# Performance work log

Hardware: AMD Instinct MI355X
Metric: run time of the kernel (lower is better)

The kernel has to match this reference:

```python
import jax, jax.numpy as jnp
import numpy as np

N_NODES = 50000
N_HYPEREDGES = 50000
E = 320000
D = 256


def _prelu(x, a):
    return jnp.where(x >= 0, x, a * x)


def _hypergraph_conv(x, hei, W, b, num_nodes, num_edges):
    # PyG HypergraphConv, use_attention=False, heads=1:
    # out = D^{-1} H B^{-1} H^T (X W^T) + b
    src = hei[0]  # node indices, [E]
    he = hei[1]   # hyperedge indices, [E]
    xw = x @ W.T  # [N, D] node transform (lin has no bias)
    ones = jnp.ones((hei.shape[1],), x.dtype)
    deg_n = jax.ops.segment_sum(ones, src, num_segments=num_nodes)   # node degree D
    deg_e = jax.ops.segment_sum(ones, he, num_segments=num_edges)    # hyperedge size B
    d_inv = jnp.where(deg_n > 0, 1.0 / deg_n, 0.0)
    b_inv = jnp.where(deg_e > 0, 1.0 / deg_e, 0.0)
    # node -> hyperedge aggregation, scaled by B^{-1}
    edge_feat = b_inv[:, None] * jax.ops.segment_sum(xw[src], he, num_segments=num_edges)  # [n_he, D]
    # hyperedge -> node aggregation, scaled by D^{-1}
    out = d_inv[:, None] * jax.ops.segment_sum(edge_feat[he], src, num_segments=num_nodes)  # [N, D]
    return out + b


def setup_inputs() -> dict:
    key = jax.random.key(0)
    ks = jax.random.split(key, 6)
    std = np.sqrt(2.0 / D)  # kaiming_normal
    x = jax.random.normal(ks[0], (N_NODES, D), dtype=jnp.float32)
    hyper_edge_index = jax.random.randint(ks[1], (2, E), 0, N_HYPEREDGES, dtype=jnp.int64)
    W1 = jax.random.normal(ks[2], (D, D), dtype=jnp.float32) * std
    b1 = jnp.zeros((D,), jnp.float32)
    W2 = jax.random.normal(ks[3], (D, D), dtype=jnp.float32) * std
    b2 = jnp.zeros((D,), jnp.float32)
    prelu_a = jnp.asarray(0.25, jnp.float32)
    return {"x": x, "W1": W1, "b1": b1, "W2": W2, "b2": b2,
            "prelu_a": prelu_a, "hyper_edge_index": hyper_edge_index}


def reference(x, W1, b1, W2, b2, prelu_a, hyper_edge_index):
    out = _hypergraph_conv(x, hyper_edge_index, W1, b1, N_NODES, N_HYPEREDGES)
    out = _prelu(out, prelu_a)
    out = _hypergraph_conv(out, hyper_edge_index, W2, b2, N_NODES, N_HYPEREDGES)
    out = out + x  # residual
    out = _prelu(out, prelu_a)
    return out
```

## Files before the change

kernel.cpp:

```cpp
#include <hip/hip_runtime.h>

#define NN    50000
#define NHE   50000
#define NEDGE 320000
#define DD    256

#define SB    1024
#define NBLK  ((NN + SB - 1) / SB)
#define CNTB  ((NEDGE / 4 + 255) / 256)
#define FB    ((NEDGE / 4 + 1023) / 1024)

typedef float f32x4 __attribute__((ext_vector_type(4)));
typedef short short8 __attribute__((ext_vector_type(8)));

static __device__ __forceinline__ unsigned short f2b(float f) {
    union { float f; unsigned u; } c; c.f = f;
    unsigned u = c.u;
    u += 0x7fffu + ((u >> 16) & 1u);
    return (unsigned short)(u >> 16);
}
static __device__ __forceinline__ float b2f_lo(unsigned v) {
    union { unsigned u; float f; } c; c.u = v << 16; return c.f;
}
static __device__ __forceinline__ float b2f_hi(unsigned v) {
    union { unsigned u; float f; } c; c.u = v & 0xffff0000u; return c.f;
}
static __device__ __forceinline__ unsigned pack2(float a, float b) {
    return (unsigned)f2b(a) | ((unsigned)f2b(b) << 16);
}

static __device__ __forceinline__ void glds16(const unsigned short* g, unsigned short* l) {
    __builtin_amdgcn_global_load_lds((const __attribute__((address_space(1))) unsigned int*)g,
                                     (__attribute__((address_space(3))) unsigned int*)l,
                                     16, 0, 0);
}

__global__ __launch_bounds__(256) void k_count_cvt(const int* __restrict__ src,
                                                   const int* __restrict__ he,
                                                   int* __restrict__ cnt_n,
                                                   int* __restrict__ cnt_e,
                                                   int* __restrict__ rank_n,
                                                   int* __restrict__ rank_e,
                                                   const float* __restrict__ w1,
                                                   const float* __restrict__ w2,
                                                   unsigned short* __restrict__ o1,
                                                   unsigned short* __restrict__ o2) {
    int bx = blockIdx.x;
    if (bx >= CNTB) {
        int t = (bx - CNTB) * 256 + threadIdx.x;
        const int n4 = DD * DD / 4;
        const float* s = (t < n4) ? w1 : w2;
        unsigned short* d = (t < n4) ? o1 : o2;
        int i = (t < n4) ? t : t - n4;
        float4 v = ((const float4*)s)[i];
        uint2 o;
        o.x = pack2(v.x, v.y);
        o.y = pack2(v.z, v.w);
        ((uint2*)d)[i] = o;
        return;
    }
    int t  = bx * 256 + threadIdx.x;
    int e0 = t * 4;
    if (e0 >= NEDGE) return;
    int4 s = *(const int4*)(src + e0);
    int4 h = *(const int4*)(he + e0);
    int4 rn, re;
    rn.x = atomicAdd(&cnt_n[s.x], 1);
    rn.y = atomicAdd(&cnt_n[s.y], 1);
    rn.z = atomicAdd(&cnt_n[s.z], 1);
    rn.w = atomicAdd(&cnt_n[s.w], 1);
    re.x = atomicAdd(&cnt_e[h.x], 1);
    re.y = atomicAdd(&cnt_e[h.y], 1);
    re.z = atomicAdd(&cnt_e[h.z], 1);
    re.w = atomicAdd(&cnt_e[h.w], 1);
    *(int4*)(rank_n + e0) = rn;
    *(int4*)(rank_e + e0) = re;
}

__global__ __launch_bounds__(256) void k_scan(const int* __restrict__ cnt_n,
                                              const int* __restrict__ cnt_e,
                                              int* __restrict__ off_n,
                                              int* __restrict__ off_e) {
    int b   = blockIdx.x;
    int seg = b / NBLK, lb = b % NBLK;
    const int* cnt = seg ? cnt_e : cnt_n;
    int* off = seg ? off_e : off_n;
    int t = threadIdx.x;

    int pre = lb * SB;
    int s = 0;
    for (int i = t * 4; i < pre; i += 1024) {
        int4 c = *(const int4*)(cnt + i);
        s += c.x + c.y + c.z + c.w;
    }
    __shared__ int red[256];
    red[t] = s;
    __syncthreads();
    for (int o = 128; o > 0; o >>= 1) {
        if (t < o) red[t] += red[t + o];
        __syncthreads();
    }
    int base = red[0];

    int idx = pre + t * 4;
    int v[4];
    int tsum = 0;
#pragma unroll
    for (int j = 0; j < 4; ++j) {
        v[j] = (idx + j < NN) ? cnt[idx + j] : 0;
        tsum += v[j];
    }
    __shared__ int sc[256];
    sc[t] = tsum;
    __syncthreads();
    for (int o = 1; o < 256; o <<= 1) {
        int val = (t >= o) ? sc[t - o] : 0;
        __syncthreads();
        sc[t] += val;
        __syncthreads();
    }
    int p = base + sc[t] - tsum;
#pragma unroll
    for (int j = 0; j < 4; ++j) {
        if (idx + j < NN) off[idx + j] = p;
        p += v[j];
    }
    if (lb == NBLK - 1 && t == 255) off[NN] = base + sc[255];
}

template <bool A32>
static __device__ __forceinline__ void gemm_bres_body(const void* __restrict__ Av,
                                                      const unsigned short* __restrict__ Wb,
                                                      unsigned short* __restrict__ Cb,
                                                      int bid) {
    __shared__ __align__(16) unsigned short Bs[128 * 256];
    const int t    = threadIdx.x;
    const int lane = t & 63;
    const int wave = t >> 6;
    const int n0   = (bid & 1) * 128;

#pragma unroll
    for (int q = 0; q < 4; ++q) {
        int row   = q * 32 + wave * 2 + (lane >> 5);
        int chunk = lane & 31;
        glds16(Wb + (size_t)(n0 + row) * DD + ((chunk ^ (row & 7)) * 8),
               Bs + q * 8192 + wave * 512);
    }
    __syncthreads();

    const int fr = lane & 15;
    const int fq = lane >> 4;
    int chunk = (bid >> 1) * 16 + wave;
    if (chunk * 16 >= NN) return;
    int m0 = chunk * 16;

    f32x4 acc[8] = {};
    short8 af[8];
    if (A32) {
        const float* p = (const float*)Av + (size_t)(m0 + fr) * DD + fq * 8;
#pragma unroll
        for (int kc = 0; kc < 8; ++kc) {
            const float* pp = p + kc * 32;
            float4 f0 = ((const float4*)pp)[0];
            float4 f1 = ((const float4*)pp)[1];
            uint4 u;
            u.x = pack2(f0.x, f0.y); u.y = pack2(f0.z, f0.w);
            u.z = pack2(f1.x, f1.y); u.w = pack2(f1.z, f1.w);
            af[kc] = *(short8*)&u;
        }
    } else {
        const unsigned short* p = (const unsigned short*)Av + (size_t)(m0 + fr) * DD + fq * 8;
#pragma unroll
        for (int kc = 0; kc < 8; ++kc)
            af[kc] = *(const short8*)(p + kc * 32);
    }

#pragma unroll
    for (int kc = 0; kc < 8; ++kc) {
#pragma unroll
        for (int nt = 0; nt < 8; ++nt) {
            int r  = nt * 16 + fr;
            int ch = (kc * 4 + fq) ^ (fr & 7);
            short8 bf = *(const short8*)(Bs + r * 256 + ch * 8);
            acc[nt] = __builtin_amdgcn_mfma_f32_16x16x32_bf16(af[kc], bf, acc[nt], 0, 0, 0);
        }
    }

#pragma unroll
    for (int nt = 0; nt < 8; ++nt)
#pragma unroll
        for (int i = 0; i < 4; ++i)
            Cb[(size_t)(m0 + fq * 4 + i) * DD + n0 + nt * 16 + fr] = f2b(acc[nt][i]);
}

__global__ __launch_bounds__(1024) void k_fill_gemm1(const int* __restrict__ src,
                                                     const int* __restrict__ he,
                                                     const int* __restrict__ off_n,
                                                     const int* __restrict__ off_e,
                                                     const int* __restrict__ rank_n,
                                                     const int* __restrict__ rank_e,
                                                     int* __restrict__ adj_n,
                                                     int* __restrict__ adj_e,
                                                     const float* __restrict__ x,
                                                     const unsigned short* __restrict__ w1b,
                                                     unsigned short* __restrict__ B1) {
    int bx = blockIdx.x;
    if (bx < FB) {
        int t  = bx * 1024 + threadIdx.x;
        int e0 = t * 4;
        if (e0 >= NEDGE) return;
        int4 s  = *(const int4*)(src + e0);
        int4 h  = *(const int4*)(he + e0);
        int4 rn = *(const int4*)(rank_n + e0);
        int4 re = *(const int4*)(rank_e + e0);
        int on0 = off_n[s.x], on1 = off_n[s.y], on2 = off_n[s.z], on3 = off_n[s.w];
        int oe0 = off_e[h.x], oe1 = off_e[h.y], oe2 = off_e[h.z], oe3 = off_e[h.w];
        adj_n[on0 + rn.x] = h.x;
        adj_n[on1 + rn.y] = h.y;
        adj_n[on2 + rn.z] = h.z;
        adj_n[on3 + rn.w] = h.w;
        adj_e[oe0 + re.x] = s.x;
        adj_e[oe1 + re.y] = s.y;
        adj_e[oe2 + re.z] = s.z;
        adj_e[oe3 + re.w] = s.w;
        return;
    }
    gemm_bres_body<true>((const void*)x, w1b, B1, bx - FB);
}

__global__ __launch_bounds__(1024) void k_gemm2(const unsigned short* __restrict__ Av,
                                                const unsigned short* __restrict__ Wb,
                                                unsigned short* __restrict__ Cb) {
    gemm_bres_body<false>((const void*)Av, Wb, Cb, blockIdx.x);
}

static __device__ __forceinline__ void acc8(float* a, uint4 v) {
    a[0] += b2f_lo(v.x); a[1] += b2f_hi(v.x);
    a[2] += b2f_lo(v.y); a[3] += b2f_hi(v.y);
    a[4] += b2f_lo(v.z); a[5] += b2f_hi(v.z);
    a[6] += b2f_lo(v.w); a[7] += b2f_hi(v.w);
}
static __device__ __forceinline__ void gather8(const unsigned short* __restrict__ srcb,
                                               const int* __restrict__ adj,
                                               int b, int e, int sl, float* a) {
#pragma unroll
    for (int i = 0; i < 8; ++i) a[i] = 0.f;
    for (int i = b; i < e; i += 8) {
        int g0 = adj[i];
        int g[8];
        g[0] = g0;
#pragma unroll
        for (int j = 1; j < 8; ++j) g[j] = (i + j < e) ? adj[i + j] : g0;
        uint4 v[8];
#pragma unroll
        for (int j = 0; j < 8; ++j)
            v[j] = *(const uint4*)(srcb + (size_t)g[j] * DD + sl * 8);
        acc8(a, v[0]);
#pragma unroll
        for (int j = 1; j < 8; ++j)
            if (i + j < e) acc8(a, v[j]);
    }
}

__global__ __launch_bounds__(256) void k_gather_edge_b(const unsigned short* __restrict__ xw,
                                                       unsigned short* __restrict__ ef,
                                                       const int* __restrict__ off,
                                                       const int* __restrict__ adj) {
    int tid = blockIdx.x * 256 + threadIdx.x;
    int w = tid >> 5;
    int sl = tid & 31;
    if (w >= NHE) return;
    int b = off[w], e = off[w + 1];
    float a[8];
    gather8(xw, adj, b, e, sl, a);
    float sc = (e > b) ? 1.f / (float)(e - b) : 0.f;
    uint4 o;
    o.x = pack2(a[0] * sc, a[1] * sc);
    o.y = pack2(a[2] * sc, a[3] * sc);
    o.z = pack2(a[4] * sc, a[5] * sc);
    o.w = pack2(a[6] * sc, a[7] * sc);
    *(uint4*)(ef + (size_t)w * DD + sl * 8) = o;
}

__global__ __launch_bounds__(256) void k_gather_node_mid_b(const unsigned short* __restrict__ ef,
                                                           unsigned short* __restrict__ h,
                                                           const int* __restrict__ off,
                                                           const int* __restrict__ adj,
                                                           const float* __restrict__ bias,
                                                           const float* __restrict__ aP) {
    int tid = blockIdx.x * 256 + threadIdx.x;
    int w = tid >> 5;
    int sl = tid & 31;
    if (w >= NN) return;
    int b = off[w], e = off[w + 1];
    float a[8];
    gather8(ef, adj, b, e, sl, a);
    float sc = (e > b) ? 1.f / (float)(e - b) : 0.f;
    float al = *aP;
    float4 bb0 = ((const float4*)bias)[sl * 2];
    float4 bb1 = ((const float4*)bias)[sl * 2 + 1];
    float r[8];
    r[0] = a[0] * sc + bb0.x; r[1] = a[1] * sc + bb0.y;
    r[2] = a[2] * sc + bb0.z; r[3] = a[3] * sc + bb0.w;
    r[4] = a[4] * sc + bb1.x; r[5] = a[5] * sc + bb1.y;
    r[6] = a[6] * sc + bb1.z; r[7] = a[7] * sc + bb1.w;
#pragma unroll
    for (int i = 0; i < 8; ++i) r[i] = (r[i] >= 0.f) ? r[i] : al * r[i];
    uint4 o;
    o.x = pack2(r[0], r[1]);
    o.y = pack2(r[2], r[3]);
    o.z = pack2(r[4], r[5]);
    o.w = pack2(r[6], r[7]);
    *(uint4*)(h + (size_t)w * DD + sl * 8) = o;
}

__global__ __launch_bounds__(256) void k_gather_node_final_b(const unsigned short* __restrict__ ef,
                                                             const float* __restrict__ x,
                                                             float* __restrict__ out,
                                                             const int* __restrict__ off,
                                                             const int* __restrict__ adj,
                                                             const float* __restrict__ bias,
                                                             const float* __restrict__ aP) {
    int tid = blockIdx.x * 256 + threadIdx.x;
    int w = tid >> 5;
    int sl = tid & 31;
    if (w >= NN) return;
    int b = off[w], e = off[w + 1];
    float a[8];
    gather8(ef, adj, b, e, sl, a);
    float sc = (e > b) ? 1.f / (float)(e - b) : 0.f;
    float al = *aP;
    float4 bb0 = ((const float4*)bias)[sl * 2];
    float4 bb1 = ((const float4*)bias)[sl * 2 + 1];
    const float* xp = x + (size_t)w * DD + sl * 8;
    float4 xv0 = *(const float4*)xp;
    float4 xv1 = *(const float4*)(xp + 4);
    float r[8];
    r[0] = a[0] * sc + bb0.x + xv0.x; r[1] = a[1] * sc + bb0.y + xv0.y;
    r[2] = a[2] * sc + bb0.z + xv0.z; r[3] = a[3] * sc + bb0.w + xv0.w;
    r[4] = a[4] * sc + bb1.x + xv1.x; r[5] = a[5] * sc + bb1.y + xv1.y;
    r[6] = a[6] * sc + bb1.z + xv1.z; r[7] = a[7] * sc + bb1.w + xv1.w;
#pragma unroll
    for (int i = 0; i < 8; ++i) r[i] = (r[i] >= 0.f) ? r[i] : al * r[i];
    float* op = out + (size_t)w * DD + sl * 8;
    *(float4*)op = make_float4(r[0], r[1], r[2], r[3]);
    *(float4*)(op + 4) = make_float4(r[4], r[5], r[6], r[7]);
}

extern "C" void kernel_launch(void* const* d_in, const int* in_sizes, int n_in,
                              void* d_out, int out_size, void* d_ws, size_t ws_size,
                              hipStream_t stream) {
    const float* x       = (const float*)d_in[0];
    const float* W1      = (const float*)d_in[1];
    const float* b1      = (const float*)d_in[2];
    const float* W2      = (const float*)d_in[3];
    const float* b2      = (const float*)d_in[4];
    const float* prelu_a = (const float*)d_in[5];
    const int*   hei     = (const int*)d_in[6];
    const int* idx_src = hei;
    const int* idx_he  = hei + NEDGE;

    float* out = (float*)d_out;
    unsigned short* B1 = (unsigned short*)d_ws;
    unsigned short* B2 = B1 + (size_t)NN * DD;
    int* off_n  = (int*)(B2 + (size_t)NN * DD);
    int* off_e  = off_n + NN + 1;
    int* cnt_n  = off_e + NHE + 1;
    int* cnt_e  = cnt_n + NN;
    int* adj_n  = cnt_e + NHE;
    int* adj_e  = adj_n + NEDGE;
    int* rank_n = adj_e + NEDGE;
    int* rank_e = rank_n + NEDGE;
    unsigned short* w1b = (unsigned short*)d_out;
    unsigned short* w2b = w1b + DD * DD;

    const int gblocks = (NN * 32 + 255) / 256;
    const int gemmb   = 2 * ((NN / 16 + 15) / 16);

    hipMemsetAsync(cnt_n, 0, sizeof(int) * (NN + NHE), stream);
    k_count_cvt<<<CNTB + 128, 256, 0, stream>>>(idx_src, idx_he, cnt_n, cnt_e,
                                                rank_n, rank_e, W1, W2, w1b, w2b);
    k_scan<<<2 * NBLK, 256, 0, stream>>>(cnt_n, cnt_e, off_n, off_e);

    k_fill_gemm1<<<FB + gemmb, 1024, 0, stream>>>(idx_src, idx_he, off_n, off_e,
                                                  rank_n, rank_e, adj_n, adj_e,
                                                  x, w1b, B1);
    k_gather_edge_b<<<gblocks, 256, 0, stream>>>(B1, B2, off_e, adj_e);
    k_gather_node_mid_b<<<gblocks, 256, 0, stream>>>(B2, B1, off_n, adj_n, b1, prelu_a);

    k_gemm2<<<gemmb, 1024, 0, stream>>>(B1, w2b, B2);
    k_gather_edge_b<<<gblocks, 256, 0, stream>>>(B2, B1, off_e, adj_e);
    k_gather_node_final_b<<<gblocks, 256, 0, stream>>>(B1, x, out, off_n, adj_n, b2, prelu_a);
}
```

Baseline: 312.7 us.

## Move x bf16 conversion into count kernel and split fill from GEMM1

The fp32-to-bf16 conversion of x now runs as extra blocks of the counting kernel, writing into the B2 workspace, so GEMM1 reads bf16 A like GEMM2 and one GEMM kernel serves both layers. The adjacency fill becomes its own 256-thread kernel instead of sharing a 1024-thread launch with GEMM1. The GEMM now issues its A-fragment loads before the LDS barrier and clamps the last row chunk so those loads stay in bounds. This adds a kernel launch and an extra pass writing and reading bf16 x, and gives up the old overlap of the fill work with GEMM1.

New measurement: 306.4 us. -2.0%, faster.

```diff
diff --git a/kernel.cpp b/kernel.cpp
--- a/kernel.cpp
+++ b/kernel.cpp
@@ -8,7 +8,7 @@
 #define SB    1024
 #define NBLK  ((NN + SB - 1) / SB)
 #define CNTB  ((NEDGE / 4 + 255) / 256)
-#define FB    ((NEDGE / 4 + 1023) / 1024)
+#define XCB   (NN * DD / 2048)
 
 typedef float f32x4 __attribute__((ext_vector_type(4)));
 typedef short short8 __attribute__((ext_vector_type(8)));
@@ -44,8 +44,20 @@
                                                    const float* __restrict__ w1,
                                                    const float* __restrict__ w2,
                                                    unsigned short* __restrict__ o1,
-                                                   unsigned short* __restrict__ o2) {
+                                                   unsigned short* __restrict__ o2,
+                                                   const float* __restrict__ x,
+                                                   unsigned short* __restrict__ xb) {
     int bx = blockIdx.x;
+    if (bx >= CNTB + 128) {
+        int t = (bx - CNTB - 128) * 256 + threadIdx.x;
+        const float4* p = (const float4*)x + (size_t)t * 2;
+        float4 a = p[0], b = p[1];
+        uint4 o;
+        o.x = pack2(a.x, a.y); o.y = pack2(a.z, a.w);
+        o.z = pack2(b.x, b.y); o.w = pack2(b.z, b.w);
+        ((uint4*)xb)[t] = o;
+        return;
+    }
     if (bx >= CNTB) {
         int t = (bx - CNTB) * 256 + threadIdx.x;
         const int n4 = DD * DD / 4;
@@ -128,16 +140,43 @@
     if (lb == NBLK - 1 && t == 255) off[NN] = base + sc[255];
 }
 
-template <bool A32>
-static __device__ __forceinline__ void gemm_bres_body(const void* __restrict__ Av,
-                                                      const unsigned short* __restrict__ Wb,
-                                                      unsigned short* __restrict__ Cb,
-                                                      int bid) {
+__global__ __launch_bounds__(256) void k_fill(const int* __restrict__ src,
+                                              const int* __restrict__ he,
+                                              const int* __restrict__ off_n,
+                                              const int* __restrict__ off_e,
+                                              const int* __restrict__ rank_n,
+                                              const int* __restrict__ rank_e,
+                                              int* __restrict__ adj_n,
+                                              int* __restrict__ adj_e) {
+    int t  = blockIdx.x * 256 + threadIdx.x;
+    int e0 = t * 4;
+    if (e0 >= NEDGE) return;
+    int4 s  = *(const int4*)(src + e0);
+    int4 h  = *(const int4*)(he + e0);
+    int4 rn = *(const int4*)(rank_n + e0);
+    int4 re = *(const int4*)(rank_e + e0);
+    int on0 = off_n[s.x], on1 = off_n[s.y], on2 = off_n[s.z], on3 = off_n[s.w];
+    int oe0 = off_e[h.x], oe1 = off_e[h.y], oe2 = off_e[h.z], oe3 = off_e[h.w];
+    adj_n[on0 + rn.x] = h.x;
+    adj_n[on1 + rn.y] = h.y;
+    adj_n[on2 + rn.z] = h.z;
+    adj_n[on3 + rn.w] = h.w;
+    adj_e[oe0 + re.x] = s.x;
+    adj_e[oe1 + re.y] = s.y;
+    adj_e[oe2 + re.z] = s.z;
+    adj_e[oe3 + re.w] = s.w;
+}
+
+__global__ __launch_bounds__(1024) void k_gemm(const unsigned short* __restrict__ Av,
+                                               const unsigned short* __restrict__ Wb,
+                                               unsigned short* __restrict__ Cb) {
     __shared__ __align__(16) unsigned short Bs[128 * 256];
     const int t    = threadIdx.x;
     const int lane = t & 63;
     const int wave = t >> 6;
-    const int n0   = (bid & 1) * 128;
+    const int n0   = (blockIdx.x & 1) * 128;
+    const int fr   = lane & 15;
+    const int fq   = lane >> 4;
 
 #pragma unroll
     for (int q = 0; q < 4; ++q) {
@@ -146,35 +185,22 @@
         glds16(Wb + (size_t)(n0 + row) * DD + ((chunk ^ (row & 7)) * 8),
                Bs + q * 8192 + wave * 512);
     }
-    __syncthreads();
-
-    const int fr = lane & 15;
-    const int fq = lane >> 4;
-    int chunk = (bid >> 1) * 16 + wave;
-    if (chunk * 16 >= NN) return;
-    int m0 = chunk * 16;
-
-    f32x4 acc[8] = {};
+
+    int mchunk = (blockIdx.x >> 1) * 16 + wave;
+    int m0  = mchunk * 16;
+    int m0c = (m0 + 16 <= NN) ? m0 : NN - 16;
     short8 af[8];
-    if (A32) {
-        const float* p = (const float*)Av + (size_t)(m0 + fr) * DD + fq * 8;
-#pragma unroll
-        for (int kc = 0; kc < 8; ++kc) {
-            const float* pp = p + kc * 32;
-            float4 f0 = ((const float4*)pp)[0];
-            float4 f1 = ((const float4*)pp)[1];
-            uint4 u;
-            u.x = pack2(f0.x, f0.y); u.y = pack2(f0.z, f0.w);
-            u.z = pack2(f1.x, f1.y); u.w = pack2(f1.z, f1.w);
-            af[kc] = *(short8*)&u;
-        }
-    } else {
-        const unsigned short* p = (const unsigned short*)Av + (size_t)(m0 + fr) * DD + fq * 8;
+    {
+        const unsigned short* p = Av + (size_t)(m0c + fr) * DD + fq * 8;
 #pragma unroll
         for (int kc = 0; kc < 8; ++kc)
             af[kc] = *(const short8*)(p + kc * 32);
     }
 
+    __syncthreads();
+    if (m0 >= NN) return;
+
+    f32x4 acc[8] = {};
 #pragma unroll
     for (int kc = 0; kc < 8; ++kc) {
 #pragma unroll
@@ -191,47 +217,6 @@
 #pragma unroll
         for (int i = 0; i < 4; ++i)
             Cb[(size_t)(m0 + fq * 4 + i) * DD + n0 + nt * 16 + fr] = f2b(acc[nt][i]);
-}
-
-__global__ __launch_bounds__(1024) void k_fill_gemm1(const int* __restrict__ src,
-                                                     const int* __restrict__ he,
-                                                     const int* __restrict__ off_n,
-                                                     const int* __restrict__ off_e,
-                                                     const int* __restrict__ rank_n,
-                                                     const int* __restrict__ rank_e,
-                                                     int* __restrict__ adj_n,
-                                                     int* __restrict__ adj_e,
-                                                     const float* __restrict__ x,
-                                                     const unsigned short* __restrict__ w1b,
-                                                     unsigned short* __restrict__ B1) {
-    int bx = blockIdx.x;
-    if (bx < FB) {
-        int t  = bx * 1024 + threadIdx.x;
-        int e0 = t * 4;
-        if (e0 >= NEDGE) return;
-        int4 s  = *(const int4*)(src + e0);
-        int4 h  = *(const int4*)(he + e0);
-        int4 rn = *(const int4*)(rank_n + e0);
-        int4 re = *(const int4*)(rank_e + e0);
-        int on0 = off_n[s.x], on1 = off_n[s.y], on2 = off_n[s.z], on3 = off_n[s.w];
-        int oe0 = off_e[h.x], oe1 = off_e[h.y], oe2 = off_e[h.z], oe3 = off_e[h.w];
-        adj_n[on0 + rn.x] = h.x;
-        adj_n[on1 + rn.y] = h.y;
-        adj_n[on2 + rn.z] = h.z;
-        adj_n[on3 + rn.w] = h.w;
-        adj_e[oe0 + re.x] = s.x;
-        adj_e[oe1 + re.y] = s.y;
-        adj_e[oe2 + re.z] = s.z;
-        adj_e[oe3 + re.w] = s.w;
-        return;
-    }
-    gemm_bres_body<true>((const void*)x, w1b, B1, bx - FB);
-}
-
-__global__ __launch_bounds__(1024) void k_gemm2(const unsigned short* __restrict__ Av,
-                                                const unsigned short* __restrict__ Wb,
-                                                unsigned short* __restrict__ Cb) {
-    gemm_bres_body<false>((const void*)Av, Wb, Cb, blockIdx.x);
 }
 
 static __device__ __forceinline__ void acc8(float* a, uint4 v) {
@@ -375,20 +360,21 @@
     unsigned short* w2b = w1b + DD * DD;
 
     const int gblocks = (NN * 32 + 255) / 256;
-    const int gemmb   = 2 * ((NN / 16 + 15) / 16);
+    const int gemmb   = 2 * (NN / 16 / 16 + 1);
 
     hipMemsetAsync(cnt_n, 0, sizeof(int) * (NN + NHE), stream);
-    k_count_cvt<<<CNTB + 128, 256, 0, stream>>>(idx_src, idx_he, cnt_n, cnt_e,
-                                                rank_n, rank_e, W1, W2, w1b, w2b);
+    k_count_cvt<<<CNTB + 128 + XCB, 256, 0, stream>>>(idx_src, idx_he, cnt_n, cnt_e,
+                                                      rank_n, rank_e, W1, W2, w1b, w2b,
+                                                      x, B2);
     k_scan<<<2 * NBLK, 256, 0, stream>>>(cnt_n, cnt_e, off_n, off_e);
-
-    k_fill_gemm1<<<FB + gemmb, 1024, 0, stream>>>(idx_src, idx_he, off_n, off_e,
-                                                  rank_n, rank_e, adj_n, adj_e,
-                                                  x, w1b, B1);
+    k_fill<<<CNTB, 256, 0, stream>>>(idx_src, idx_he, off_n, off_e,
+                                     rank_n, rank_e, adj_n, adj_e);
+
+    k_gemm<<<gemmb, 1024, 0, stream>>>(B2, w1b, B1);
     k_gather_edge_b<<<gblocks, 256, 0, stream>>>(B1, B2, off_e, adj_e);
     k_gather_node_mid_b<<<gblocks, 256, 0, stream>>>(B2, B1, off_n, adj_n, b1, prelu_a);
 
-    k_gemm2<<<gemmb, 1024, 0, stream>>>(B1, w2b, B2);
+    k_gemm<<<gemmb, 1024, 0, stream>>>(B1, w2b, B2);
     k_gather_edge_b<<<gblocks, 256, 0, stream>>>(B2, B1, off_e, adj_e);
     k_gather_node_final_b<<<gblocks, 256, 0, stream>>>(B1, x, out, off_n, adj_n, b2, prelu_a);
 }
```
